# Kernel optimization log

Hardware: AMD Instinct MI355X
Metric: run time of the kernel (lower is better)

## Reference

```python
import jax, jax.numpy as jnp
import numpy as np
from jax import lax

RADIUS = (3, 3, 3)  # box-filter kernel size per spatial axis (named 'radius' in source)
EPS = 1e-6


def box_sum_3d(x, ksizes=RADIUS):
    # Separable box-filter local SUM, equivalent to conv3d with an all-ones
    # (1,1,3,3,3) kernel and padding='same'.
    for ax_idx, k in enumerate(ksizes):
        kshape = [1, 1, 1, 1, 1]
        kshape[2 + ax_idx] = k
        kern = jnp.ones(kshape, dtype=x.dtype)
        x = lax.conv_general_dilated(
            x, kern, window_strides=(1, 1, 1), padding='SAME',
            dimension_numbers=('NCDHW', 'OIDHW', 'NCDHW'))
    return x


def image_gradient_3d(image):
    # torch.gradient: central differences interior, one-sided at boundaries.
    gz, gy, gx = jnp.gradient(image, axis=(2, 3, 4))
    return jnp.concatenate([gz, gy, gx], axis=1)  # [B,3,D,H,W]


def setup_inputs() -> dict:
    key = jax.random.key(0)
    k1, k2, k3, k4 = jax.random.split(key, 4)
    shape = (1, 1, 256, 256, 256)
    moving_image = jax.random.normal(k1, shape, dtype=jnp.float32)
    fixed_image = jax.random.normal(k2, shape, dtype=jnp.float32)
    moving_mask = jax.random.bernoulli(k3, 0.5, shape)
    fixed_mask = jax.random.bernoulli(k4, 0.5, shape)
    return {"moving_image": moving_image, "fixed_image": fixed_image,
            "moving_mask": moving_mask, "fixed_mask": fixed_mask}


def reference(moving_image, fixed_image, moving_mask, fixed_mask):
    npix = float(np.prod(RADIUS))  # 27

    sum_m = box_sum_3d(moving_image)
    sum_f = box_sum_3d(fixed_image)
    sum_mm = box_sum_3d(moving_image * moving_image)
    sum_ff = box_sum_3d(fixed_image * fixed_image)
    sum_mf = box_sum_3d(moving_image * fixed_image)

    moving_mean = sum_m / npix
    fixed_mean = sum_f / npix

    var_m = sum_mm - 2 * moving_mean * sum_m + npix * moving_mean * moving_mean
    var_f = sum_ff - 2 * fixed_mean * sum_f + npix * fixed_mean * fixed_mean
    var_mf = var_m * var_f
    cross = sum_mf - fixed_mean * sum_m - moving_mean * sum_f + npix * moving_mean * fixed_mean

    # dual-force total gradient: masked moving grad + masked fixed grad, halved
    grad_moving = image_gradient_3d(moving_image) * moving_mask.astype(moving_image.dtype)
    grad_fixed = image_gradient_3d(fixed_image) * fixed_mask.astype(fixed_image.dtype)
    total_grad = (grad_moving + grad_fixed) * 0.5  # [B,3,D,H,W]

    moving_mean_centered = moving_image - moving_mean
    fixed_mean_centered = fixed_image - fixed_mean
    factor = (2.0 * cross / (var_mf + EPS)
              * (moving_mean_centered - cross / (var_f * fixed_mean_centered + EPS)))

    # (cross_correlation / metric are only printed in the original, not returned)
    return -1.0 * factor * total_grad
```

## Files before the change

### kernel.cpp

```cpp
#include <hip/hip_runtime.h>


constexpr int DIM     = 256;
constexpr int PLANE   = DIM * DIM;
constexpr int NVOX    = DIM * DIM * DIM;
constexpr int CHUNK_Z = 8;
constexpr int BY      = 2;
constexpr float EPSF  = 1e-6f;

typedef float nvec4 __attribute__((ext_vector_type(4)));
typedef int   nivec4 __attribute__((ext_vector_type(4)));

__device__ __forceinline__ float shlz(float v) {
    float r = __shfl_up(v, 1);
    return (threadIdx.x == 0) ? 0.f : r;
}
__device__ __forceinline__ float shrz(float v) {
    float r = __shfl_down(v, 1);
    return (threadIdx.x == 63) ? 0.f : r;
}
__device__ __forceinline__ float4 add3(const float4& a, const float4& b, const float4& c) {
    return make_float4(a.x+b.x+c.x, a.y+b.y+c.y, a.z+b.z+c.z, a.w+b.w+c.w);
}
__device__ __forceinline__ float4 prod3(const float4& a, const float4& b,
                                        const float4& c, const float4& d,
                                        const float4& e, const float4& f) {
    return make_float4(a.x*b.x + c.x*d.x + e.x*f.x,
                       a.y*b.y + c.y*d.y + e.y*f.y,
                       a.z*b.z + c.z*d.z + e.z*f.z,
                       a.w*b.w + c.w*d.w + e.w*f.w);
}
__device__ __forceinline__ float4 sub4(const float4& a, const float4& b) {
    return make_float4(a.x-b.x, a.y-b.y, a.z-b.z, a.w-b.w);
}
__device__ __forceinline__ float4 scl4(const float4& a, float s) {
    return make_float4(a.x*s, a.y*s, a.z*s, a.w*s);
}
__device__ __forceinline__ float4 xsum3(const float4& c) {
    float l = shlz(c.w), r = shrz(c.x);
    return make_float4(l + c.x + c.y, c.x + c.y + c.z, c.y + c.z + c.w, c.z + c.w + r);
}
__device__ __forceinline__ void ntstore4(float* p, const float4& v) {
    nvec4 t; t.x = v.x; t.y = v.y; t.z = v.z; t.w = v.w;
    __builtin_nontemporal_store(t, (nvec4*)p);
}

__device__ __forceinline__ void pw1(
    float sum_m, float sum_f, float sum_mm, float sum_ff, float sum_mf,
    float mA, float mB, float mN,
    float fA, float fB, float fN,
    int zflag,
    float gx_m, float gy_m, float gx_f, float gy_f,
    int km, int kf,
    float& o0, float& o1, float& o2)
{
    float mmean = sum_m / 27.0f;
    float fmean = sum_f / 27.0f;
    float var_m = sum_mm - 2.f*mmean*sum_m + 27.f*mmean*mmean;
    float var_f = sum_ff - 2.f*fmean*sum_f + 27.f*fmean*fmean;
    float var_mf = var_m * var_f;
    float cross = sum_mf - fmean*sum_m - mmean*sum_f + 27.f*mmean*fmean;
    float mmc = mB - mmean, fmc = fB - fmean;
    float factor = 2.f * cross / (var_mf + EPSF)
                   * (mmc - cross / (var_f*fmc + EPSF));
    float gzm = (zflag < 0) ? (mN - mB) : ((zflag > 0) ? (mB - mA) : 0.5f*(mN - mA));
    float gzf = (zflag < 0) ? (fN - fB) : ((zflag > 0) ? (fB - fA) : 0.5f*(fN - fA));
    float wm = km ? 1.f : 0.f, wf = kf ? 1.f : 0.f;
    float tgz = 0.5f*(gzm *wm + gzf *wf);
    float tgy = 0.5f*(gy_m*wm + gy_f*wf);
    float tgx = 0.5f*(gx_m*wm + gx_f*wf);
    o0 = -factor * tgz;
    o1 = -factor * tgy;
    o2 = -factor * tgx;
}

__global__ __launch_bounds__(64 * BY) void ncc_forces(
    const float* __restrict__ M, const float* __restrict__ F,
    const int* __restrict__ maskM, const int* __restrict__ maskF,
    float* __restrict__ out)
{
    const int y  = blockIdx.y * BY + threadIdx.y;
    const int z0 = blockIdx.z * CHUNK_Z;
    const int xb = threadIdx.x * 4;
    const bool yUok = (y > 0), yDok = (y < DIM - 1);

    float4 Pm[3], Pf[3], Pmm[3], Pff[3], Pmf[3];
    float4 mc[3], fc[3];
    float4 gxm_p, gym_p, gxf_p, gyf_p;

    auto ingest = [&](int slot, int zl, float4& gxm, float4& gym, float4& gxf, float4& gyf) {
        const float4 z4 = make_float4(0.f, 0.f, 0.f, 0.f);
        float4 mU = z4, mC = z4, mD = z4, fU = z4, fC = z4, fD = z4;
        if ((unsigned)zl < (unsigned)DIM) {
            const float* pm = M + (size_t)zl * PLANE + (size_t)y * DIM + xb;
            const float* pf = F + (size_t)zl * PLANE + (size_t)y * DIM + xb;
            mC = *(const float4*)pm;  fC = *(const float4*)pf;
            if (yUok) { mU = *(const float4*)(pm - DIM); fU = *(const float4*)(pf - DIM); }
            if (yDok) { mD = *(const float4*)(pm + DIM); fD = *(const float4*)(pf + DIM); }
        }
        float4 Cm  = add3(mU, mC, mD);
        float4 Cf  = add3(fU, fC, fD);
        float4 Cmm = prod3(mU, mU, mC, mC, mD, mD);
        float4 Cff = prod3(fU, fU, fC, fC, fD, fD);
        float4 Cmf = prod3(mU, fU, mC, fC, mD, fD);
        Pm[slot]  = xsum3(Cm);
        Pf[slot]  = xsum3(Cf);
        Pmm[slot] = xsum3(Cmm);
        Pff[slot] = xsum3(Cff);
        Pmf[slot] = xsum3(Cmf);
        mc[slot] = mC; fc[slot] = fC;
        float mL = shlz(mC.w), mR = shrz(mC.x);
        float fL = shlz(fC.w), fR = shrz(fC.x);
        gxm = make_float4((threadIdx.x == 0)  ? (mC.y - mC.x) : 0.5f*(mC.y - mL),
                          0.5f*(mC.z - mC.x),
                          0.5f*(mC.w - mC.y),
                          (threadIdx.x == 63) ? (mC.w - mC.z) : 0.5f*(mR - mC.z));
        gxf = make_float4((threadIdx.x == 0)  ? (fC.y - fC.x) : 0.5f*(fC.y - fL),
                          0.5f*(fC.z - fC.x),
                          0.5f*(fC.w - fC.y),
                          (threadIdx.x == 63) ? (fC.w - fC.z) : 0.5f*(fR - fC.z));
        gym = (y == 0) ? sub4(mD, mC) : (y == DIM-1) ? sub4(mC, mU) : scl4(sub4(mD, mU), 0.5f);
        gyf = (y == 0) ? sub4(fD, fC) : (y == DIM-1) ? sub4(fC, fU) : scl4(sub4(fD, fU), 0.5f);
    };

    { float4 d0, d1, d2, d3; ingest(0, z0 - 1, d0, d1, d2, d3); }
    ingest(1, z0, gxm_p, gym_p, gxf_p, gyf_p);

    #pragma unroll
    for (int s = 2; s < CHUNK_Z + 2; ++s) {
        const int i2 = s % 3, i1 = (s + 2) % 3, i0 = (s + 1) % 3;
        float4 gxm, gym, gxf, gyf;
        ingest(i2, z0 - 1 + s, gxm, gym, gxf, gyf);

        const int zo = z0 + s - 2;
        const int zflag = (zo == 0) ? -1 : ((zo == DIM - 1) ? 1 : 0);
        const size_t idx = (size_t)zo * PLANE + (size_t)y * DIM + xb;

        nivec4 km = __builtin_nontemporal_load((const nivec4*)(maskM + idx));
        nivec4 kf = __builtin_nontemporal_load((const nivec4*)(maskF + idx));

        float4 sm  = add3(Pm[i0],  Pm[i1],  Pm[i2]);
        float4 sf  = add3(Pf[i0],  Pf[i1],  Pf[i2]);
        float4 smm = add3(Pmm[i0], Pmm[i1], Pmm[i2]);
        float4 sff = add3(Pff[i0], Pff[i1], Pff[i2]);
        float4 smf = add3(Pmf[i0], Pmf[i1], Pmf[i2]);

        float4 o0, o1, o2;
        pw1(sm.x, sf.x, smm.x, sff.x, smf.x, mc[i0].x, mc[i1].x, mc[i2].x,
            fc[i0].x, fc[i1].x, fc[i2].x, zflag, gxm_p.x, gym_p.x, gxf_p.x, gyf_p.x,
            km.x, kf.x, o0.x, o1.x, o2.x);
        pw1(sm.y, sf.y, smm.y, sff.y, smf.y, mc[i0].y, mc[i1].y, mc[i2].y,
            fc[i0].y, fc[i1].y, fc[i2].y, zflag, gxm_p.y, gym_p.y, gxf_p.y, gyf_p.y,
            km.y, kf.y, o0.y, o1.y, o2.y);
        pw1(sm.z, sf.z, smm.z, sff.z, smf.z, mc[i0].z, mc[i1].z, mc[i2].z,
            fc[i0].z, fc[i1].z, fc[i2].z, zflag, gxm_p.z, gym_p.z, gxf_p.z, gyf_p.z,
            km.z, kf.z, o0.z, o1.z, o2.z);
        pw1(sm.w, sf.w, smm.w, sff.w, smf.w, mc[i0].w, mc[i1].w, mc[i2].w,
            fc[i0].w, fc[i1].w, fc[i2].w, zflag, gxm_p.w, gym_p.w, gxf_p.w, gyf_p.w,
            km.w, kf.w, o0.w, o1.w, o2.w);

        ntstore4(out + idx,            o0);
        ntstore4(out + NVOX + idx,     o1);
        ntstore4(out + 2 * NVOX + idx, o2);

        gxm_p = gxm; gym_p = gym; gxf_p = gxf; gyf_p = gyf;
    }
}

extern "C" void kernel_launch(void* const* d_in, const int* in_sizes, int n_in,
                              void* d_out, int out_size, void* d_ws, size_t ws_size,
                              hipStream_t stream) {
    const float* M  = (const float*)d_in[0];
    const float* F  = (const float*)d_in[1];
    const int* mm   = (const int*)d_in[2];
    const int* fm   = (const int*)d_in[3];
    float* out      = (float*)d_out;

    dim3 block(64, BY, 1);
    dim3 grid(1, DIM / BY, DIM / CHUNK_Z);
    hipLaunchKernelGGL(ncc_forces, grid, block, 0, stream, M, F, mm, fm, out);
}
```

Baseline: 384.8 us.

## Software-prefetch next z-plane and masks, keep running partial sums for z-window

Splits plane ingestion into a load stage and a compute stage, so the next z-plane's image rows and mask values are issued one iteration ahead and their latency overlaps the current plane's arithmetic. The three-slot partial-sum arrays are replaced by two running pair sums, which removes one add per quantity per output. It also sets a minimum of 4 blocks per CU in launch_bounds. The cost is higher register pressure from the in-flight prefetch registers, which may force spills under the occupancy constraint.

Result: slower. 584.4 us (+51.9%).

```diff
diff --git a/kernel.cpp b/kernel.cpp
--- a/kernel.cpp
+++ b/kernel.cpp
@@ -21,6 +21,9 @@
 }
 __device__ __forceinline__ float4 add3(const float4& a, const float4& b, const float4& c) {
     return make_float4(a.x+b.x+c.x, a.y+b.y+c.y, a.z+b.z+c.z, a.w+b.w+c.w);
+}
+__device__ __forceinline__ float4 add2(const float4& a, const float4& b) {
+    return make_float4(a.x+b.x, a.y+b.y, a.z+b.z, a.w+b.w);
 }
 __device__ __forceinline__ float4 prod3(const float4& a, const float4& b,
                                         const float4& c, const float4& d,
@@ -74,7 +77,58 @@
     o2 = -factor * tgx;
 }
 
-__global__ __launch_bounds__(64 * BY) void ncc_forces(
+struct RawP { float4 mU, mC, mD, fU, fC, fD; };
+
+__device__ __forceinline__ RawP load_planes(const float* __restrict__ M,
+                                            const float* __restrict__ F,
+                                            int zl, size_t yoff, bool yUok, bool yDok)
+{
+    const float4 z4 = make_float4(0.f, 0.f, 0.f, 0.f);
+    RawP r; r.mU = z4; r.mC = z4; r.mD = z4; r.fU = z4; r.fC = z4; r.fD = z4;
+    if ((unsigned)zl < (unsigned)DIM) {
+        const float* pm = M + (size_t)zl * PLANE + yoff;
+        const float* pf = F + (size_t)zl * PLANE + yoff;
+        r.mC = *(const float4*)pm;  r.fC = *(const float4*)pf;
+        if (yUok) { r.mU = *(const float4*)(pm - DIM); r.fU = *(const float4*)(pf - DIM); }
+        if (yDok) { r.mD = *(const float4*)(pm + DIM); r.fD = *(const float4*)(pf + DIM); }
+    }
+    return r;
+}
+
+__device__ __forceinline__ void ingest_compute(
+    const RawP& r, int slot, int y,
+    float4* mc, float4* fc,
+    float4& Pm, float4& Pf, float4& Pmm, float4& Pff, float4& Pmf,
+    float4& gxm, float4& gym, float4& gxf, float4& gyf)
+{
+    const float4 mU = r.mU, mC = r.mC, mD = r.mD;
+    const float4 fU = r.fU, fC = r.fC, fD = r.fD;
+    float4 Cm  = add3(mU, mC, mD);
+    float4 Cf  = add3(fU, fC, fD);
+    float4 Cmm = prod3(mU, mU, mC, mC, mD, mD);
+    float4 Cff = prod3(fU, fU, fC, fC, fD, fD);
+    float4 Cmf = prod3(mU, fU, mC, fC, mD, fD);
+    Pm  = xsum3(Cm);
+    Pf  = xsum3(Cf);
+    Pmm = xsum3(Cmm);
+    Pff = xsum3(Cff);
+    Pmf = xsum3(Cmf);
+    mc[slot] = mC; fc[slot] = fC;
+    float mL = shlz(mC.w), mR = shrz(mC.x);
+    float fL = shlz(fC.w), fR = shrz(fC.x);
+    gxm = make_float4((threadIdx.x == 0)  ? (mC.y - mC.x) : 0.5f*(mC.y - mL),
+                      0.5f*(mC.z - mC.x),
+                      0.5f*(mC.w - mC.y),
+                      (threadIdx.x == 63) ? (mC.w - mC.z) : 0.5f*(mR - mC.z));
+    gxf = make_float4((threadIdx.x == 0)  ? (fC.y - fC.x) : 0.5f*(fC.y - fL),
+                      0.5f*(fC.z - fC.x),
+                      0.5f*(fC.w - fC.y),
+                      (threadIdx.x == 63) ? (fC.w - fC.z) : 0.5f*(fR - fC.z));
+    gym = (y == 0) ? sub4(mD, mC) : (y == DIM-1) ? sub4(mC, mU) : scl4(sub4(mD, mU), 0.5f);
+    gyf = (y == 0) ? sub4(fD, fC) : (y == DIM-1) ? sub4(fC, fU) : scl4(sub4(fD, fU), 0.5f);
+}
+
+__global__ __launch_bounds__(64 * BY, 4) void ncc_forces(
     const float* __restrict__ M, const float* __restrict__ F,
     const int* __restrict__ maskM, const int* __restrict__ maskF,
     float* __restrict__ out)
@@ -83,67 +137,55 @@
     const int z0 = blockIdx.z * CHUNK_Z;
     const int xb = threadIdx.x * 4;
     const bool yUok = (y > 0), yDok = (y < DIM - 1);
-
-    float4 Pm[3], Pf[3], Pmm[3], Pff[3], Pmf[3];
+    const size_t yoff = (size_t)y * DIM + xb;
+
     float4 mc[3], fc[3];
     float4 gxm_p, gym_p, gxf_p, gyf_p;
 
-    auto ingest = [&](int slot, int zl, float4& gxm, float4& gym, float4& gxf, float4& gyf) {
-        const float4 z4 = make_float4(0.f, 0.f, 0.f, 0.f);
-        float4 mU = z4, mC = z4, mD = z4, fU = z4, fC = z4, fD = z4;
-        if ((unsigned)zl < (unsigned)DIM) {
-            const float* pm = M + (size_t)zl * PLANE + (size_t)y * DIM + xb;
-            const float* pf = F + (size_t)zl * PLANE + (size_t)y * DIM + xb;
-            mC = *(const float4*)pm;  fC = *(const float4*)pf;
-            if (yUok) { mU = *(const float4*)(pm - DIM); fU = *(const float4*)(pf - DIM); }
-            if (yDok) { mD = *(const float4*)(pm + DIM); fD = *(const float4*)(pf + DIM); }
-        }
-        float4 Cm  = add3(mU, mC, mD);
-        float4 Cf  = add3(fU, fC, fD);
-        float4 Cmm = prod3(mU, mU, mC, mC, mD, mD);
-        float4 Cff = prod3(fU, fU, fC, fC, fD, fD);
-        float4 Cmf = prod3(mU, fU, mC, fC, mD, fD);
-        Pm[slot]  = xsum3(Cm);
-        Pf[slot]  = xsum3(Cf);
-        Pmm[slot] = xsum3(Cmm);
-        Pff[slot] = xsum3(Cff);
-        Pmf[slot] = xsum3(Cmf);
-        mc[slot] = mC; fc[slot] = fC;
-        float mL = shlz(mC.w), mR = shrz(mC.x);
-        float fL = shlz(fC.w), fR = shrz(fC.x);
-        gxm = make_float4((threadIdx.x == 0)  ? (mC.y - mC.x) : 0.5f*(mC.y - mL),
-                          0.5f*(mC.z - mC.x),
-                          0.5f*(mC.w - mC.y),
-                          (threadIdx.x == 63) ? (mC.w - mC.z) : 0.5f*(mR - mC.z));
-        gxf = make_float4((threadIdx.x == 0)  ? (fC.y - fC.x) : 0.5f*(fC.y - fL),
-                          0.5f*(fC.z - fC.x),
-                          0.5f*(fC.w - fC.y),
-                          (threadIdx.x == 63) ? (fC.w - fC.z) : 0.5f*(fR - fC.z));
-        gym = (y == 0) ? sub4(mD, mC) : (y == DIM-1) ? sub4(mC, mU) : scl4(sub4(mD, mU), 0.5f);
-        gyf = (y == 0) ? sub4(fD, fC) : (y == DIM-1) ? sub4(fC, fU) : scl4(sub4(fD, fU), 0.5f);
-    };
-
-    { float4 d0, d1, d2, d3; ingest(0, z0 - 1, d0, d1, d2, d3); }
-    ingest(1, z0, gxm_p, gym_p, gxf_p, gyf_p);
+    nivec4 km = __builtin_nontemporal_load((const nivec4*)(maskM + (size_t)z0 * PLANE + yoff));
+    nivec4 kf = __builtin_nontemporal_load((const nivec4*)(maskF + (size_t)z0 * PLANE + yoff));
+    RawP r0 = load_planes(M, F, z0 - 1, yoff, yUok, yDok);
+    RawP r1 = load_planes(M, F, z0,     yoff, yUok, yDok);
+    RawP rN = load_planes(M, F, z0 + 1, yoff, yUok, yDok);
+
+    float4 SAm, SAf, SAmm, SAff, SAmf, SBm, SBf, SBmm, SBff, SBmf;
+    {
+        float4 P0m, P0f, P0mm, P0ff, P0mf, d0, d1, d2, d3;
+        ingest_compute(r0, 0, y, mc, fc, P0m, P0f, P0mm, P0ff, P0mf, d0, d1, d2, d3);
+        float4 P1m, P1f, P1mm, P1ff, P1mf;
+        ingest_compute(r1, 1, y, mc, fc, P1m, P1f, P1mm, P1ff, P1mf,
+                       gxm_p, gym_p, gxf_p, gyf_p);
+        SAm  = add2(P0m,  P1m );  SBm  = P1m;
+        SAf  = add2(P0f,  P1f );  SBf  = P1f;
+        SAmm = add2(P0mm, P1mm);  SBmm = P1mm;
+        SAff = add2(P0ff, P1ff);  SBff = P1ff;
+        SAmf = add2(P0mf, P1mf);  SBmf = P1mf;
+    }
 
     #pragma unroll
     for (int s = 2; s < CHUNK_Z + 2; ++s) {
         const int i2 = s % 3, i1 = (s + 2) % 3, i0 = (s + 1) % 3;
-        float4 gxm, gym, gxf, gyf;
-        ingest(i2, z0 - 1 + s, gxm, gym, gxf, gyf);
-
         const int zo = z0 + s - 2;
         const int zflag = (zo == 0) ? -1 : ((zo == DIM - 1) ? 1 : 0);
-        const size_t idx = (size_t)zo * PLANE + (size_t)y * DIM + xb;
-
-        nivec4 km = __builtin_nontemporal_load((const nivec4*)(maskM + idx));
-        nivec4 kf = __builtin_nontemporal_load((const nivec4*)(maskF + idx));
-
-        float4 sm  = add3(Pm[i0],  Pm[i1],  Pm[i2]);
-        float4 sf  = add3(Pf[i0],  Pf[i1],  Pf[i2]);
-        float4 smm = add3(Pmm[i0], Pmm[i1], Pmm[i2]);
-        float4 sff = add3(Pff[i0], Pff[i1], Pff[i2]);
-        float4 smf = add3(Pmf[i0], Pmf[i1], Pmf[i2]);
+        const size_t idx = (size_t)zo * PLANE + yoff;
+
+        float4 gxm, gym, gxf, gyf;
+        float4 Pm2, Pf2, Pmm2, Pff2, Pmf2;
+        ingest_compute(rN, i2, y, mc, fc, Pm2, Pf2, Pmm2, Pff2, Pmf2,
+                       gxm, gym, gxf, gyf);
+
+        nivec4 kmT, kfT;
+        if (s < CHUNK_Z + 1) {
+            rN  = load_planes(M, F, z0 + s, yoff, yUok, yDok);
+            kmT = __builtin_nontemporal_load((const nivec4*)(maskM + idx + PLANE));
+            kfT = __builtin_nontemporal_load((const nivec4*)(maskF + idx + PLANE));
+        }
+
+        float4 sm  = add2(SAm,  Pm2);
+        float4 sf  = add2(SAf,  Pf2);
+        float4 smm = add2(SAmm, Pmm2);
+        float4 sff = add2(SAff, Pff2);
+        float4 smf = add2(SAmf, Pmf2);
 
         float4 o0, o1, o2;
         pw1(sm.x, sf.x, smm.x, sff.x, smf.x, mc[i0].x, mc[i1].x, mc[i2].x,
@@ -163,7 +205,13 @@
         ntstore4(out + NVOX + idx,     o1);
         ntstore4(out + 2 * NVOX + idx, o2);
 
+        SAm  = add2(SBm,  Pm2 );  SBm  = Pm2;
+        SAf  = add2(SBf,  Pf2 );  SBf  = Pf2;
+        SAmm = add2(SBmm, Pmm2);  SBmm = Pmm2;
+        SAff = add2(SBff, Pff2);  SBff = Pff2;
+        SAmf = add2(SBmf, Pmf2);  SBmf = Pmf2;
         gxm_p = gxm; gym_p = gym; gxf_p = gxf; gyf_p = gyf;
+        if (s < CHUNK_Z + 1) { km = kmT; kf = kfT; }
     }
 }
 
```
